# Kernel tuning notes

Measured on AMD Instinct MI355X. Metric: run time of the kernel, lower is better.

Reference implementation:

```python
import jax, jax.numpy as jnp
import numpy as np

Z_DIM = 256
N_MOD = 8
CAT = Z_DIM * N_MOD          # 2048
YS = 1024
B = 4096
EPS = 1e-5


def _layer_norm(x, g, b):
    mu = jnp.mean(x, axis=-1, keepdims=True)
    var = jnp.mean((x - mu) ** 2, axis=-1, keepdims=True)
    return (x - mu) * jax.lax.rsqrt(var + EPS) * g + b


def setup_inputs() -> dict:
    key = jax.random.key(0)
    ks = jax.random.split(key, 16)
    s_cat = 1.0 / np.sqrt(CAT)
    s_ys = 1.0 / np.sqrt(YS)
    return {
        "z_stack": jax.random.normal(ks[0], (N_MOD, B, Z_DIM), jnp.float32),
        "Wq": jax.random.normal(ks[1], (CAT, CAT), jnp.float32) * s_cat,
        "bq": jnp.zeros((CAT,), jnp.float32),
        "Wk": jax.random.normal(ks[2], (CAT, CAT), jnp.float32) * s_cat,
        "bk": jnp.zeros((CAT,), jnp.float32),
        "Wv": jax.random.normal(ks[3], (CAT, CAT), jnp.float32) * s_cat,
        "bv": jnp.zeros((CAT,), jnp.float32),
        "W1": jax.random.normal(ks[4], (CAT, YS), jnp.float32) * s_cat,
        "b1": jnp.zeros((YS,), jnp.float32),
        "W2": jax.random.normal(ks[5], (YS, CAT), jnp.float32) * s_ys,
        "b2": jnp.zeros((CAT,), jnp.float32),
        "ln1_g": jnp.ones((CAT,), jnp.float32),
        "ln1_b": jnp.zeros((CAT,), jnp.float32),
        "ln2_g": jnp.ones((CAT,), jnp.float32),
        "ln2_b": jnp.zeros((CAT,), jnp.float32),
        "Wys": jax.random.normal(ks[6], (CAT, YS), jnp.float32) * s_cat,
        "bys": jnp.zeros((YS,), jnp.float32),
        "Ws": jax.random.normal(ks[7], (N_MOD, YS, Z_DIM), jnp.float32) * s_ys,
        "bs": jnp.zeros((N_MOD, Z_DIM), jnp.float32),
    }


def reference(z_stack, Wq, bq, Wk, bk, Wv, bv, W1, b1, W2, b2,
              ln1_g, ln1_b, ln2_g, ln2_b, Wys, bys, Ws, bs):
    M, Bn, Zd = z_stack.shape
    # torch.cat(z, dim=1): [B, M*Zd]
    x = jnp.transpose(z_stack, (1, 0, 2)).reshape(Bn, M * Zd)
    # self-attention over the batch dim (unscaled, as in source)
    q = x @ Wq + bq
    k = x @ Wk + bk
    v = x @ Wv + bv
    attended = jax.nn.softmax(q @ k.T, axis=-1) @ v  # [B, B] scores
    # dropout is identity in eval mode
    x = _layer_norm(x + attended, ln1_g, ln1_b)
    h = jax.nn.gelu(x @ W1 + b1, approximate=False) @ W2 + b2
    h = _layer_norm(x + h, ln2_g, ln2_b)
    yb = h @ Wys + bys                               # [B, YS]
    # per-module scaling layers, stacked output [M, B, Zd]
    y = jnp.einsum('bs,msz->mbz', yb, Ws) + bs[:, None, :]
    return y
```

## Files before the change

kernel.cpp:

```cpp
#include <hip/hip_runtime.h>
#include <hip/hip_bf16.h>
#include <cstdint>
#include <cstddef>
#include <math.h>

typedef __bf16 bf16x8 __attribute__((ext_vector_type(8)));
typedef float  f32x4  __attribute__((ext_vector_type(4)));

#define DEVI __device__ __forceinline__

static constexpr int BB = 4096;
static constexpr int CD = 2048;
static constexpr int ZD = 256;

DEVI unsigned short f2bf(float f) {
  __bf16 h = (__bf16)f;
  return __builtin_bit_cast(unsigned short, h);
}
DEVI float bf2f(unsigned short u) {
  return (float)__builtin_bit_cast(__bf16, u);
}

DEVI void gload_lds16(const void* g, void* l) {
  __builtin_amdgcn_global_load_lds(
      (__attribute__((address_space(1))) void*)(g),
      (__attribute__((address_space(3))) void*)(l), 16, 0, 0);
}

DEVI int swz(int L) { return L ^ (((L >> 7) & 7) << 4); }

__global__ __launch_bounds__(256) void pack_x(
    const float* __restrict__ z, float* __restrict__ x,
    unsigned short* __restrict__ x2) {
  const int i = (blockIdx.x * 256 + threadIdx.x) * 4;
  const int m  = i >> 20;
  const int r  = i & 1048575;
  const int b  = r >> 8;
  const int zd = r & 255;
  const float4 v = *(const float4*)(z + i);
  const size_t o32 = (size_t)b * CD + m * ZD + zd;
  *(float4*)(x + o32) = v;
  ushort4 h, l;
  h.x = f2bf(v.x); l.x = f2bf(v.x - bf2f(h.x));
  h.y = f2bf(v.y); l.y = f2bf(v.y - bf2f(h.y));
  h.z = f2bf(v.z); l.z = f2bf(v.z - bf2f(h.z));
  h.w = f2bf(v.w); l.w = f2bf(v.w - bf2f(h.w));
  const size_t o2 = (size_t)b * 4096 + m * ZD + zd;
  *(ushort4*)(x2 + o2) = h;
  *(ushort4*)(x2 + o2 + 2048) = l;
}

template<bool LO>
__global__ void transpose_split(const float* __restrict__ in,
                                unsigned short* __restrict__ oh,
                                int R, int C, int ldo) {
  __shared__ float tile[32][33];
  const int c0 = blockIdx.x * 32, r0 = blockIdx.y * 32;
  const int tx = threadIdx.x, ty = threadIdx.y;
#pragma unroll
  for (int k = 0; k < 4; ++k)
    tile[ty + 8 * k][tx] = in[(size_t)(r0 + ty + 8 * k) * C + (c0 + tx)];
  __syncthreads();
#pragma unroll
  for (int k = 0; k < 4; ++k) {
    const float f = tile[tx][ty + 8 * k];
    const size_t o = (size_t)(c0 + ty + 8 * k) * ldo + (r0 + tx);
    const unsigned short h = f2bf(f);
    oh[o] = h;
    if constexpr (LO) oh[o + R] = f2bf(f - bf2f(h));
  }
}

__global__ void transpose_ws(const float* __restrict__ in,
                             unsigned short* __restrict__ outp) {
  __shared__ float tile[32][33];
  const int m = blockIdx.z;
  const float* src = in + (size_t)m * 262144;
  unsigned short* dst = outp + (size_t)m * 262144;
  const int c0 = blockIdx.x * 32, r0 = blockIdx.y * 32;
  const int tx = threadIdx.x, ty = threadIdx.y;
#pragma unroll
  for (int k = 0; k < 4; ++k)
    tile[ty + 8 * k][tx] = src[(size_t)(r0 + ty + 8 * k) * 256 + (c0 + tx)];
  __syncthreads();
#pragma unroll
  for (int k = 0; k < 4; ++k)
    dst[(size_t)(c0 + ty + 8 * k) * 1024 + (r0 + tx)] = f2bf(tile[tx][ty + 8 * k]);
}

__global__ void transpose_bf16(const unsigned short* __restrict__ in,
                               unsigned short* __restrict__ outp, int R, int C) {
  __shared__ unsigned short tile[32][33];
  const int c0 = blockIdx.x * 32, r0 = blockIdx.y * 32;
  const int tx = threadIdx.x, ty = threadIdx.y;
#pragma unroll
  for (int k = 0; k < 4; ++k)
    tile[ty + 8 * k][tx] = in[(size_t)(r0 + ty + 8 * k) * C + (c0 + tx)];
  __syncthreads();
#pragma unroll
  for (int k = 0; k < 4; ++k)
    outp[(size_t)(c0 + ty + 8 * k) * R + (r0 + tx)] = tile[tx][ty + 8 * k];
}

#define DOMFMA(QI, QJ, AF, BF)                                            \
  {                                                                       \
    _Pragma("unroll") for (int ks = 0; ks < 2; ++ks) {                    \
      _Pragma("unroll") for (int f = 0; f < 4; ++f) {                     \
        _Pragma("unroll") for (int g = 0; g < 2; ++g) {                   \
          acc[(QI) * 4 + f][(QJ) * 2 + g] =                               \
              __builtin_amdgcn_mfma_f32_16x16x32_bf16(                    \
                  AF[f][ks], BF[g][ks], acc[(QI) * 4 + f][(QJ) * 2 + g],  \
                  0, 0, 0);                                               \
        }                                                                 \
      }                                                                   \
    }                                                                     \
  }

#define PH_SYNC()                                         \
  do {                                                    \
    __builtin_amdgcn_s_barrier();                         \
    asm volatile("s_waitcnt lgkmcnt(0)" ::: "memory");    \
    __builtin_amdgcn_sched_barrier(0);                    \
    __builtin_amdgcn_s_setprio(1);                        \
  } while (0)

#define PH_END()                                          \
  do {                                                    \
    __builtin_amdgcn_s_setprio(0);                        \
    __builtin_amdgcn_sched_barrier(0);                    \
    __builtin_amdgcn_s_barrier();                         \
  } while (0)

template<int EP, bool SEG>
__global__ __launch_bounds__(512, 2) void gemm256(
    const unsigned short* __restrict__ A,
    const unsigned short* __restrict__ Bt,
    const float* __restrict__ bias, const float* __restrict__ bias2,
    float* __restrict__ Cf,
    unsigned short* __restrict__ Ob1, unsigned short* __restrict__ Ob2,
    int Kv, int lda, int ldb, int N, int nbx) {
  extern __shared__ char lds[];
  const int NK = Kv >> 6;
  const int t = threadIdx.x;
  const int lane = t & 63;
  const int w = t >> 6;
  const int wm = w >> 2, wn = w & 3;
  const int lr = lane & 15, kg = lane >> 4;
  const int q8 = gridDim.x >> 3;
  const int bid = (blockIdx.x & 7) * q8 + (blockIdx.x >> 3);
  const int bx = bid % nbx, by = bid / nbx;
  const int Ar0 = by * 256, Br0 = bx * 256;

  const int Lb = t << 4;
  const int rowL = Lb >> 7;
  const int colb = swz(Lb) & 127;
  const char* Abase = (const char*)A + (size_t)(Ar0 + rowL) * lda * 2 + colb;
  const char* Bbase = (const char*)Bt + (size_t)(Br0 + rowL) * ldb * 2 + colb;
  const size_t ldaB = (size_t)lda * 128;
  const size_t ldbB = (size_t)ldb * 128;
  char* const ldw = lds + ((t >> 6) << 10);

  auto stageA = [&](int c, int kk, int dst_off) {
    gload_lds16(Abase + (size_t)c * ldaB + ((unsigned)kk << 1), ldw + dst_off);
  };
  auto stageB = [&](int c, int kk, int dst_off) {
    gload_lds16(Bbase + (size_t)c * ldbB + ((unsigned)kk << 1), ldw + dst_off);
  };
  auto rdA = [&](const char* buf, int qi, int f, int ks) {
    const int L = swz(((qi * 64 + f * 16 + lr) << 7) + ks * 64 + kg * 16);
    return *(const bf16x8*)(buf + wm * 16384 + L);
  };
  auto rdB = [&](const char* buf, int qj, int g, int ks) {
    const int L = swz(((wn * 64 + qj * 32 + g * 16 + lr) << 7) + ks * 64 + kg * 16);
    return *(const bf16x8*)(buf + 32768 + L);
  };
  auto kA = [](int k0) { return SEG ? (k0 - ((k0 >> 11) == 2 ? 4096 : 0)) : k0; };
  auto kB = [](int k0) { return SEG ? (k0 - ((k0 >> 11) >= 1 ? 2048 : 0)) : k0; };

  f32x4 acc[8][4] = {};
  bf16x8 af[4][2], b0[2][2], b1[2][2];

  {
    stageA(0, kA(0), 0);
    stageA(1, kA(0), 8192);
    stageA(2, kA(0), 16384);
    stageA(3, kA(0), 24576);
    stageB(0, kB(0), 32768);
    stageB(1, kB(0), 40960);
    stageB(2, kB(0), 49152);
    stageB(3, kB(0), 57344);
    stageA(0, kA(64), 65536 + 0);
    stageA(2, kA(64), 65536 + 16384);
    stageB(0, kB(64), 65536 + 32768);
    stageB(1, kB(64), 65536 + 40960);
    stageB(2, kB(64), 65536 + 49152);
    stageB(3, kB(64), 65536 + 57344);
    asm volatile("s_waitcnt vmcnt(6)" ::: "memory");
    __builtin_amdgcn_sched_barrier(0);
    __builtin_amdgcn_s_barrier();
  }

  for (int tt = 0; tt < NK; ++tt) {
    const int cur = tt & 1;
    const char* buf = lds + cur * 65536;
    const int curo = cur * 65536, nxto = (cur ^ 1) * 65536;
    const int k1 = (tt + 1) * 64, k2 = (tt + 2) * 64;

#pragma unroll
    for (int f = 0; f < 4; ++f)
#pragma unroll
      for (int ks = 0; ks < 2; ++ks) af[f][ks] = rdA(buf, 0, f, ks);
#pragma unroll
    for (int g = 0; g < 2; ++g)
#pragma unroll
      for (int ks = 0; ks < 2; ++ks) b0[g][ks] = rdB(buf, 0, g, ks);
    if (tt + 1 < NK) {
      stageA(1, kA(k1), nxto + 8192);
      stageA(3, kA(k1), nxto + 24576);
    }
    asm volatile("s_waitcnt lgkmcnt(8)" ::: "memory");
    __builtin_amdgcn_sched_barrier(0);
    PH_SYNC();
    DOMFMA(0, 0, af, b0);
    PH_END();

#pragma unroll
    for (int g = 0; g < 2; ++g)
#pragma unroll
      for (int ks = 0; ks < 2; ++ks) b1[g][ks] = rdB(buf, 1, g, ks);
    if (tt + 2 < NK) {
      stageA(0, kA(k2), curo + 0);
      stageA(2, kA(k2), curo + 16384);
    }
    PH_SYNC();
    DOMFMA(0, 1, af, b1);
    PH_END();

#pragma unroll
    for (int f = 0; f < 4; ++f)
#pragma unroll
      for (int ks = 0; ks < 2; ++ks) af[f][ks] = rdA(buf, 1, f, ks);
    if (tt + 2 < NK) {
      stageB(0, kB(k2), curo + 32768);
      stageB(1, kB(k2), curo + 40960);
    }
    PH_SYNC();
    DOMFMA(1, 0, af, b0);
    PH_END();

    if (tt + 2 < NK) {
      stageB(2, kB(k2), curo + 49152);
      stageB(3, kB(k2), curo + 57344);
      asm volatile("s_waitcnt vmcnt(6)" ::: "memory");
    } else {
      asm volatile("s_waitcnt vmcnt(0)" ::: "memory");
    }
    __builtin_amdgcn_sched_barrier(0);
    PH_SYNC();
    DOMFMA(1, 1, af, b1);
    PH_END();
  }

  const int rbase = Ar0 + wm * 128 + kg * 4;
  const int cbase = Br0 + wn * 64 + lr;
#pragma unroll
  for (int rf = 0; rf < 8; ++rf) {
#pragma unroll
    for (int cf = 0; cf < 4; ++cf) {
      const int col = cbase + cf * 16;
#pragma unroll
      for (int q = 0; q < 4; ++q) {
        const int row = rbase + rf * 16 + q;
        float val = acc[rf][cf][q];
        if constexpr (EP == 0) {
          Cf[(size_t)row * N + col] = val;
        } else {
          if (col < 2048) {
            val += bias[col];
            const unsigned short h = f2bf(val);
            Ob1[(size_t)row * 4096 + col] = h;
            Ob1[(size_t)row * 4096 + 2048 + col] = f2bf(val - bf2f(h));
          } else {
            const int c2 = col - 2048;
            val += bias2[c2];
            const unsigned short h = f2bf(val);
            Ob2[(size_t)row * 4096 + c2] = h;
            Ob2[(size_t)row * 4096 + 2048 + c2] = f2bf(val - bf2f(h));
          }
        }
      }
    }
  }
}

template<int EP>
__global__ __launch_bounds__(256) void gemm_bt(
    const unsigned short* __restrict__ Ah,
    const unsigned short* __restrict__ Bh,
    const float* __restrict__ bias,
    float* __restrict__ Cf, unsigned short* __restrict__ Cb,
    int M, int N, int K, int lda, int ldb) {
  __shared__ unsigned short lds[2][128 * 32];
  const int t = threadIdx.x;
  const int lane = t & 63;
  const int w = t >> 6;
  const int wr = (w >> 1) * 64, wc = (w & 1) * 64;
  const int lr = lane & 15, kg = lane >> 4;
  const size_t Ar0 = (size_t)blockIdx.y * 128;
  const size_t Br0 = (size_t)blockIdx.x * 128;

  f32x4 acc[4][4] = {};

  for (int k0 = 0; k0 < K; k0 += 32) {
#pragma unroll
    for (int rnd = 0; rnd < 2; ++rnd) {
      const int e = t * 8 + rnd * 2048;
      const int row = e >> 5, col = e & 31;
      const size_t ga = (Ar0 + row) * (size_t)lda + (k0 + col);
      const size_t gb = (Br0 + row) * (size_t)ldb + (k0 + col);
      const int lo = (w << 9) + rnd * 2048;
      gload_lds16(Ah + ga, &lds[0][lo]);
      gload_lds16(Bh + gb, &lds[1][lo]);
    }
    __syncthreads();
    bf16x8 ah[4], bh[4];
#pragma unroll
    for (int i = 0; i < 4; ++i) {
      ah[i] = *(const bf16x8*)&lds[0][((wr + i * 16 + lr) << 5) + (kg << 3)];
      bh[i] = *(const bf16x8*)&lds[1][((wc + i * 16 + lr) << 5) + (kg << 3)];
    }
#pragma unroll
    for (int i = 0; i < 4; ++i)
#pragma unroll
      for (int j = 0; j < 4; ++j)
        acc[i][j] = __builtin_amdgcn_mfma_f32_16x16x32_bf16(ah[i], bh[j], acc[i][j], 0, 0, 0);
    __syncthreads();
  }

  const int rb = (int)Ar0 + wr + (lane >> 4) * 4;
  const int cb = (int)Br0 + wc + lr;
#pragma unroll
  for (int i = 0; i < 4; ++i) {
#pragma unroll
    for (int j = 0; j < 4; ++j) {
      const int col = cb + j * 16;
      const float bsv = bias ? bias[col] : 0.0f;
#pragma unroll
      for (int q = 0; q < 4; ++q) {
        const int row = rb + i * 16 + q;
        const float val = acc[i][j][q] + bsv;
        const size_t o = (size_t)row * N + col;
        if constexpr (EP == 0) {
          Cf[o] = val;
        } else if constexpr (EP == 1) {
          Cb[o] = f2bf(val);
        } else if constexpr (EP == 2) {
          const float ge = 0.5f * val * (1.0f + erff(val * 0.70710678118654752f));
          Cb[o] = f2bf(ge);
        } else {
          const size_t oo = (size_t)(col >> 8) * ((size_t)BB * ZD)
                          + (size_t)row * ZD + (col & 255);
          Cf[oo] = val;
        }
      }
    }
  }
}

__global__ __launch_bounds__(256) void softmax_rows(const float* __restrict__ S,
                                                    unsigned short* __restrict__ P) {
  const int row = blockIdx.x;
  const int t = threadIdx.x;
  const int lane = t & 63, w = t >> 6;
  const float* s = S + (size_t)row * 4096;
  float4 v[4];
  float mx = -3.4e38f;
#pragma unroll
  for (int i = 0; i < 4; ++i) {
    v[i] = *(const float4*)(s + (size_t)(t + 256 * i) * 4);
    mx = fmaxf(mx, fmaxf(fmaxf(v[i].x, v[i].y), fmaxf(v[i].z, v[i].w)));
  }
#pragma unroll
  for (int off = 32; off >= 1; off >>= 1) mx = fmaxf(mx, __shfl_xor(mx, off));
  __shared__ float redm[4], redsum[4];
  if (lane == 0) redm[w] = mx;
  __syncthreads();
  mx = fmaxf(fmaxf(redm[0], redm[1]), fmaxf(redm[2], redm[3]));
  float sum = 0.f;
#pragma unroll
  for (int i = 0; i < 4; ++i) {
    v[i].x = expf(v[i].x - mx);
    v[i].y = expf(v[i].y - mx);
    v[i].z = expf(v[i].z - mx);
    v[i].w = expf(v[i].w - mx);
    sum += v[i].x + v[i].y + v[i].z + v[i].w;
  }
#pragma unroll
  for (int off = 32; off >= 1; off >>= 1) sum += __shfl_xor(sum, off);
  if (lane == 0) redsum[w] = sum;
  __syncthreads();
  sum = redsum[0] + redsum[1] + redsum[2] + redsum[3];
  const float inv = 1.0f / sum;
  unsigned short* p = P + (size_t)row * 4096;
#pragma unroll
  for (int i = 0; i < 4; ++i) {
    ushort4 u;
    u.x = f2bf(v[i].x * inv);
    u.y = f2bf(v[i].y * inv);
    u.z = f2bf(v[i].z * inv);
    u.w = f2bf(v[i].w * inv);
    *(ushort4*)(p + (size_t)(t + 256 * i) * 4) = u;
  }
}

template<bool WF32>
__global__ __launch_bounds__(256) void ln_fused(
    const float* __restrict__ a, const float* __restrict__ b,
    const float* __restrict__ g, const float* __restrict__ be,
    float* __restrict__ of, unsigned short* __restrict__ ob) {
  const int row = blockIdx.x;
  const int t = threadIdx.x;
  const int lane = t & 63, w = t >> 6;
  const float* ar = a + (size_t)row * 2048;
  const float* br = b + (size_t)row * 2048;
  float4 x[2];
  float s = 0.f, ss = 0.f;
#pragma unroll
  for (int i = 0; i < 2; ++i) {
    const int o = (t + 256 * i) * 4;
    const float4 av = *(const float4*)(ar + o);
    const float4 bv = *(const float4*)(br + o);
    x[i].x = av.x + bv.x; x[i].y = av.y + bv.y;
    x[i].z = av.z + bv.z; x[i].w = av.w + bv.w;
    s  += x[i].x + x[i].y + x[i].z + x[i].w;
    ss += x[i].x * x[i].x + x[i].y * x[i].y + x[i].z * x[i].z + x[i].w * x[i].w;
  }
#pragma unroll
  for (int off = 32; off >= 1; off >>= 1) {
    s  += __shfl_xor(s, off);
    ss += __shfl_xor(ss, off);
  }
  __shared__ float rs[4], rss[4];
  if (lane == 0) { rs[w] = s; rss[w] = ss; }
  __syncthreads();
  s  = rs[0] + rs[1] + rs[2] + rs[3];
  ss = rss[0] + rss[1] + rss[2] + rss[3];
  const float mu  = s * (1.0f / 2048.0f);
  const float var = ss * (1.0f / 2048.0f) - mu * mu;
  const float inv = rsqrtf(var + 1e-5f);
#pragma unroll
  for (int i = 0; i < 2; ++i) {
    const int o = (t + 256 * i) * 4;
    const float4 gv  = *(const float4*)(g + o);
    const float4 bev = *(const float4*)(be + o);
    float4 y;
    y.x = (x[i].x - mu) * inv * gv.x + bev.x;
    y.y = (x[i].y - mu) * inv * gv.y + bev.y;
    y.z = (x[i].z - mu) * inv * gv.z + bev.z;
    y.w = (x[i].w - mu) * inv * gv.w + bev.w;
    if constexpr (WF32) *(float4*)(of + (size_t)row * 2048 + o) = y;
    ushort4 u;
    u.x = f2bf(y.x); u.y = f2bf(y.y); u.z = f2bf(y.z); u.w = f2bf(y.w);
    *(ushort4*)(ob + (size_t)row * 2048 + o) = u;
  }
}

extern "C" void kernel_launch(void* const* d_in, const int* in_sizes, int n_in,
                              void* d_out, int out_size, void* d_ws, size_t ws_size,
                              hipStream_t stream) {
  (void)in_sizes; (void)n_in; (void)out_size;
  const float* z    = (const float*)d_in[0];
  const float* Wq   = (const float*)d_in[1];
  const float* bq   = (const float*)d_in[2];
  const float* Wk   = (const float*)d_in[3];
  const float* bk   = (const float*)d_in[4];
  const float* Wv   = (const float*)d_in[5];
  const float* bv   = (const float*)d_in[6];
  const float* W1   = (const float*)d_in[7];
  const float* b1   = (const float*)d_in[8];
  const float* W2   = (const float*)d_in[9];
  const float* b2   = (const float*)d_in[10];
  const float* ln1g = (const float*)d_in[11];
  const float* ln1b = (const float*)d_in[12];
  const float* ln2g = (const float*)d_in[13];
  const float* ln2b = (const float*)d_in[14];
  const float* Wys  = (const float*)d_in[15];
  const float* bys  = (const float*)d_in[16];
  const float* Ws   = (const float*)d_in[17];
  const float* bs   = (const float*)d_in[18];
  float* out = (float*)d_out;
  char* ws = (char*)d_ws;

  const size_t MB = 1048576;
  const size_t off_x    = 0;
  const size_t off_h2   = 0;
  const size_t off_x2   = 32 * MB;
  const size_t off_Bqk  = 64 * MB;
  const size_t off_S    = 32 * MB;
  const size_t off_Aq   = 96 * MB;
  const size_t off_P    = 96 * MB;
  const size_t off_x1f  = 96 * MB;
  const size_t off_Btk  = 128 * MB;
  const size_t off_att  = 128 * MB;
  const size_t off_hmid = 128 * MB;
  const size_t off_ybbf = 136 * MB;
  const size_t off_Vbf  = 160 * MB;
  const size_t off_x1bf = 160 * MB;
  const size_t off_Vt   = 176 * MB;
  const size_t off_x2bf = 176 * MB;
  const size_t off_Wvt  = 192 * MB;
  const size_t off_W1t  = 200 * MB;
  const size_t off_W2t  = 204 * MB;
  const size_t off_Wyst = 208 * MB;
  const size_t off_Wst  = 212 * MB;
  if (ws_size < 216 * MB) return;

#define F32P(o) ((float*)(ws + (o)))
#define BFP(o)  ((unsigned short*)(ws + (o)))

  const dim3 tb(32, 8);
  const int LDSB = 131072;

  pack_x<<<8192, 256, 0, stream>>>(z, F32P(off_x), BFP(off_x2));
  transpose_split<true ><<<dim3(64, 64), tb, 0, stream>>>(Wq, BFP(off_Bqk), 2048, 2048, 4096);
  transpose_split<true ><<<dim3(64, 64), tb, 0, stream>>>(Wk, BFP(off_Bqk) + (size_t)2048 * 4096, 2048, 2048, 4096);
  transpose_split<false><<<dim3(64, 64), tb, 0, stream>>>(Wv, BFP(off_Wvt), 2048, 2048, 2048);
  transpose_split<false><<<dim3(32, 64), tb, 0, stream>>>(W1, BFP(off_W1t), 2048, 1024, 2048);
  transpose_split<false><<<dim3(64, 32), tb, 0, stream>>>(W2, BFP(off_W2t), 1024, 2048, 1024);
  transpose_split<false><<<dim3(32, 64), tb, 0, stream>>>(Wys, BFP(off_Wyst), 2048, 1024, 2048);
  transpose_ws<<<dim3(8, 32, 8), tb, 0, stream>>>(Ws, BFP(off_Wst));

  gemm_bt<1><<<dim3(16, 32), 256, 0, stream>>>(BFP(off_x2), BFP(off_Wvt), bv,
      nullptr, BFP(off_Vbf), 4096, 2048, 2048, 4096, 2048);
  transpose_bf16<<<dim3(64, 128), tb, 0, stream>>>(BFP(off_Vbf), BFP(off_Vt), 4096, 2048);

  gemm256<1, true ><<<256, 512, LDSB, stream>>>(BFP(off_x2), BFP(off_Bqk), bq, bk,
      nullptr, BFP(off_Aq), BFP(off_Btk), 6144, 4096, 4096, 4096, 16);

  gemm256<0, true ><<<256, 512, LDSB, stream>>>(BFP(off_Aq), BFP(off_Btk), nullptr, nullptr,
      F32P(off_S), nullptr, nullptr, 6144, 4096, 4096, 4096, 16);

  softmax_rows<<<4096, 256, 0, stream>>>(F32P(off_S), BFP(off_P));
  gemm_bt<0><<<dim3(16, 32), 256, 0, stream>>>(BFP(off_P), BFP(off_Vt), nullptr,
      F32P(off_att), nullptr, 4096, 2048, 4096, 4096, 4096);
  ln_fused<true ><<<4096, 256, 0, stream>>>(F32P(off_x), F32P(off_att), ln1g, ln1b,
      F32P(off_x1f), BFP(off_x1bf));

  gemm_bt<2><<<dim3(8, 32), 256, 0, stream>>>(BFP(off_x1bf), BFP(off_W1t), b1,
      nullptr, BFP(off_hmid), 4096, 1024, 2048, 2048, 2048);
  gemm_bt<0><<<dim3(16, 32), 256, 0, stream>>>(BFP(off_hmid), BFP(off_W2t), b2,
      F32P(off_h2), nullptr, 4096, 2048, 1024, 1024, 1024);
  ln_fused<false><<<4096, 256, 0, stream>>>(F32P(off_x1f), F32P(off_h2), ln2g, ln2b,
      nullptr, BFP(off_x2bf));

  gemm_bt<1><<<dim3(8, 32), 256, 0, stream>>>(BFP(off_x2bf), BFP(off_Wyst), bys,
      nullptr, BFP(off_ybbf), 4096, 1024, 2048, 2048, 2048);
  gemm_bt<4><<<dim3(16, 32), 256, 0, stream>>>(BFP(off_ybbf), BFP(off_Wst), bs,
      out, nullptr, 4096, 2048, 1024, 1024, 1024);
}
```

Baseline: 785.9 us.

## Merge weight transposes, compute V transposed directly, drop fp32 x copy, remap tiles

```diff
diff --git a/kernel.cpp b/kernel.cpp
--- a/kernel.cpp
+++ b/kernel.cpp
@@ -10,7 +10,6 @@
 #define DEVI __device__ __forceinline__
 
 static constexpr int BB = 4096;
-static constexpr int CD = 2048;
 static constexpr int ZD = 256;
 
 DEVI unsigned short f2bf(float f) {
@@ -30,16 +29,13 @@
 DEVI int swz(int L) { return L ^ (((L >> 7) & 7) << 4); }
 
 __global__ __launch_bounds__(256) void pack_x(
-    const float* __restrict__ z, float* __restrict__ x,
-    unsigned short* __restrict__ x2) {
+    const float* __restrict__ z, unsigned short* __restrict__ x2) {
   const int i = (blockIdx.x * 256 + threadIdx.x) * 4;
   const int m  = i >> 20;
   const int r  = i & 1048575;
   const int b  = r >> 8;
   const int zd = r & 255;
   const float4 v = *(const float4*)(z + i);
-  const size_t o32 = (size_t)b * CD + m * ZD + zd;
-  *(float4*)(x + o32) = v;
   ushort4 h, l;
   h.x = f2bf(v.x); l.x = f2bf(v.x - bf2f(h.x));
   h.y = f2bf(v.y); l.y = f2bf(v.y - bf2f(h.y));
@@ -50,56 +46,49 @@
   *(ushort4*)(x2 + o2 + 2048) = l;
 }
 
-template<bool LO>
-__global__ void transpose_split(const float* __restrict__ in,
-                                unsigned short* __restrict__ oh,
-                                int R, int C, int ldo) {
+__global__ __launch_bounds__(256) void transpose_all(
+    const float* __restrict__ Wq, const float* __restrict__ Wk,
+    const float* __restrict__ Wv, const float* __restrict__ W1,
+    const float* __restrict__ W2, const float* __restrict__ Wys,
+    const float* __restrict__ Ws,
+    unsigned short* __restrict__ Bqk, unsigned short* __restrict__ Wvt,
+    unsigned short* __restrict__ W1t, unsigned short* __restrict__ W2t,
+    unsigned short* __restrict__ Wyst, unsigned short* __restrict__ Wst) {
   __shared__ float tile[32][33];
-  const int c0 = blockIdx.x * 32, r0 = blockIdx.y * 32;
+  int b = blockIdx.x;
+  const float* src;
+  unsigned short* dh;
+  int C, ldo, nbx, loff = 0;
+  if (b < 8192) {
+    const int which = b >> 12; b &= 4095;
+    src = which ? Wk : Wq;
+    dh = Bqk + (size_t)which * 2048 * 4096;
+    C = 2048; ldo = 4096; nbx = 64; loff = 2048;
+  } else if (b < 12288) { b -= 8192;  src = Wv;  dh = Wvt;  C = 2048; ldo = 2048; nbx = 64; }
+  else if (b < 14336)   { b -= 12288; src = W1;  dh = W1t;  C = 1024; ldo = 2048; nbx = 32; }
+  else if (b < 16384)   { b -= 14336; src = W2;  dh = W2t;  C = 2048; ldo = 1024; nbx = 64; }
+  else if (b < 18432)   { b -= 16384; src = Wys; dh = Wyst; C = 1024; ldo = 2048; nbx = 32; }
+  else {
+    b -= 18432;
+    const int m = b >> 8; b &= 255;
+    src = Ws + (size_t)m * 262144;
+    dh = Wst + (size_t)m * 262144;
+    C = 256; ldo = 1024; nbx = 8;
+  }
+  const int c0 = (b % nbx) * 32, r0 = (b / nbx) * 32;
   const int tx = threadIdx.x, ty = threadIdx.y;
 #pragma unroll
   for (int k = 0; k < 4; ++k)
-    tile[ty + 8 * k][tx] = in[(size_t)(r0 + ty + 8 * k) * C + (c0 + tx)];
+    tile[ty + 8 * k][tx] = src[(size_t)(r0 + ty + 8 * k) * C + (c0 + tx)];
   __syncthreads();
 #pragma unroll
   for (int k = 0; k < 4; ++k) {
     const float f = tile[tx][ty + 8 * k];
     const size_t o = (size_t)(c0 + ty + 8 * k) * ldo + (r0 + tx);
     const unsigned short h = f2bf(f);
-    oh[o] = h;
-    if constexpr (LO) oh[o + R] = f2bf(f - bf2f(h));
-  }
-}
-
-__global__ void transpose_ws(const float* __restrict__ in,
-                             unsigned short* __restrict__ outp) {
-  __shared__ float tile[32][33];
-  const int m = blockIdx.z;
-  const float* src = in + (size_t)m * 262144;
-  unsigned short* dst = outp + (size_t)m * 262144;
-  const int c0 = blockIdx.x * 32, r0 = blockIdx.y * 32;
-  const int tx = threadIdx.x, ty = threadIdx.y;
-#pragma unroll
-  for (int k = 0; k < 4; ++k)
-    tile[ty + 8 * k][tx] = src[(size_t)(r0 + ty + 8 * k) * 256 + (c0 + tx)];
-  __syncthreads();
-#pragma unroll
-  for (int k = 0; k < 4; ++k)
-    dst[(size_t)(c0 + ty + 8 * k) * 1024 + (r0 + tx)] = f2bf(tile[tx][ty + 8 * k]);
-}
-
-__global__ void transpose_bf16(const unsigned short* __restrict__ in,
-                               unsigned short* __restrict__ outp, int R, int C) {
-  __shared__ unsigned short tile[32][33];
-  const int c0 = blockIdx.x * 32, r0 = blockIdx.y * 32;
-  const int tx = threadIdx.x, ty = threadIdx.y;
-#pragma unroll
-  for (int k = 0; k < 4; ++k)
-    tile[ty + 8 * k][tx] = in[(size_t)(r0 + ty + 8 * k) * C + (c0 + tx)];
-  __syncthreads();
-#pragma unroll
-  for (int k = 0; k < 4; ++k)
-    outp[(size_t)(c0 + ty + 8 * k) * R + (r0 + tx)] = tile[tx][ty + 8 * k];
+    dh[o] = h;
+    if (loff) dh[o + loff] = f2bf(f - bf2f(h));
+  }
 }
 
 #define DOMFMA(QI, QJ, AF, BF)                                            \
@@ -146,9 +135,16 @@
   const int w = t >> 6;
   const int wm = w >> 2, wn = w & 3;
   const int lr = lane & 15, kg = lane >> 4;
-  const int q8 = gridDim.x >> 3;
-  const int bid = (blockIdx.x & 7) * q8 + (blockIdx.x >> 3);
-  const int bx = bid % nbx, by = bid / nbx;
+  int bx, by;
+  if (gridDim.x == 256 && nbx == 16) {
+    const int xcd = blockIdx.x & 7, i = blockIdx.x >> 3;
+    by = (xcd >> 1) * 4 + (i >> 3);
+    bx = (xcd & 1) * 8 + (i & 7);
+  } else {
+    const int q8 = gridDim.x >> 3;
+    const int bid = (blockIdx.x & 7) * q8 + (blockIdx.x >> 3);
+    bx = bid % nbx; by = bid / nbx;
+  }
   const int Ar0 = by * 256, Br0 = bx * 256;
 
   const int Lb = t << 4;
@@ -344,7 +340,7 @@
 #pragma unroll
     for (int j = 0; j < 4; ++j) {
       const int col = cb + j * 16;
-      const float bsv = bias ? bias[col] : 0.0f;
+      const float bsv = (EP == 5) ? 0.0f : (bias ? bias[col] : 0.0f);
 #pragma unroll
       for (int q = 0; q < 4; ++q) {
         const int row = rb + i * 16 + q;
@@ -357,10 +353,12 @@
         } else if constexpr (EP == 2) {
           const float ge = 0.5f * val * (1.0f + erff(val * 0.70710678118654752f));
           Cb[o] = f2bf(ge);
-        } else {
+        } else if constexpr (EP == 4) {
           const size_t oo = (size_t)(col >> 8) * ((size_t)BB * ZD)
                           + (size_t)row * ZD + (col & 255);
           Cf[oo] = val;
+        } else {
+          Cb[o] = f2bf(val + bias[row]);
         }
       }
     }
@@ -413,7 +411,7 @@
   }
 }
 
-template<bool WF32>
+template<bool ZG, bool WF32>
 __global__ __launch_bounds__(256) void ln_fused(
     const float* __restrict__ a, const float* __restrict__ b,
     const float* __restrict__ g, const float* __restrict__ be,
@@ -421,14 +419,18 @@
   const int row = blockIdx.x;
   const int t = threadIdx.x;
   const int lane = t & 63, w = t >> 6;
-  const float* ar = a + (size_t)row * 2048;
   const float* br = b + (size_t)row * 2048;
   float4 x[2];
   float s = 0.f, ss = 0.f;
 #pragma unroll
   for (int i = 0; i < 2; ++i) {
     const int o = (t + 256 * i) * 4;
-    const float4 av = *(const float4*)(ar + o);
+    float4 av;
+    if constexpr (ZG) {
+      av = *(const float4*)(a + ((size_t)(o >> 8) * 4096 + row) * 256 + (o & 255));
+    } else {
+      av = *(const float4*)(a + (size_t)row * 2048 + o);
+    }
     const float4 bv = *(const float4*)(br + o);
     x[i].x = av.x + bv.x; x[i].y = av.y + bv.y;
     x[i].z = av.z + bv.z; x[i].w = av.w + bv.w;
@@ -492,7 +494,6 @@
   char* ws = (char*)d_ws;
 
   const size_t MB = 1048576;
-  const size_t off_x    = 0;
   const size_t off_h2   = 0;
   const size_t off_x2   = 32 * MB;
   const size_t off_Bqk  = 64 * MB;
@@ -504,7 +505,6 @@
   const size_t off_att  = 128 * MB;
   const size_t off_hmid = 128 * MB;
   const size_t off_ybbf = 136 * MB;
-  const size_t off_Vbf  = 160 * MB;
   const size_t off_x1bf = 160 * MB;
   const size_t off_Vt   = 176 * MB;
   const size_t off_x2bf = 176 * MB;
@@ -518,21 +518,14 @@
 #define F32P(o) ((float*)(ws + (o)))
 #define BFP(o)  ((unsigned short*)(ws + (o)))
 
-  const dim3 tb(32, 8);
   const int LDSB = 131072;
 
-  pack_x<<<8192, 256, 0, stream>>>(z, F32P(off_x), BFP(off_x2));
-  transpose_split<true ><<<dim3(64, 64), tb, 0, stream>>>(Wq, BFP(off_Bqk), 2048, 2048, 4096);
-  transpose_split<true ><<<dim3(64, 64), tb, 0, stream>>>(Wk, BFP(off_Bqk) + (size_t)2048 * 4096, 2048, 2048, 4096);
-  transpose_split<false><<<dim3(64, 64), tb, 0, stream>>>(Wv, BFP(off_Wvt), 2048, 2048, 2048);
-  transpose_split<false><<<dim3(32, 64), tb, 0, stream>>>(W1, BFP(off_W1t), 2048, 1024, 2048);
-  transpose_split<false><<<dim3(64, 32), tb, 0, stream>>>(W2, BFP(off_W2t), 1024, 2048, 1024);
-  transpose_split<false><<<dim3(32, 64), tb, 0, stream>>>(Wys, BFP(off_Wyst), 2048, 1024, 2048);
-  transpose_ws<<<dim3(8, 32, 8), tb, 0, stream>>>(Ws, BFP(off_Wst));
-
-  gemm_bt<1><<<dim3(16, 32), 256, 0, stream>>>(BFP(off_x2), BFP(off_Wvt), bv,
-      nullptr, BFP(off_Vbf), 4096, 2048, 2048, 4096, 2048);
-  transpose_bf16<<<dim3(64, 128), tb, 0, stream>>>(BFP(off_Vbf), BFP(off_Vt), 4096, 2048);
+  pack_x<<<8192, 256, 0, stream>>>(z, BFP(off_x2));
+  transpose_all<<<20480, dim3(32, 8), 0, stream>>>(Wq, Wk, Wv, W1, W2, Wys, Ws,
+      BFP(off_Bqk), BFP(off_Wvt), BFP(off_W1t), BFP(off_W2t), BFP(off_Wyst), BFP(off_Wst));
+
+  gemm_bt<5><<<dim3(32, 16), 256, 0, stream>>>(BFP(off_Wvt), BFP(off_x2), bv,
+      nullptr, BFP(off_Vt), 2048, 4096, 2048, 2048, 4096);
 
   gemm256<1, true ><<<256, 512, LDSB, stream>>>(BFP(off_x2), BFP(off_Bqk), bq, bk,
       nullptr, BFP(off_Aq), BFP(off_Btk), 6144, 4096, 4096, 4096, 16);
@@ -543,14 +536,14 @@
   softmax_rows<<<4096, 256, 0, stream>>>(F32P(off_S), BFP(off_P));
   gemm_bt<0><<<dim3(16, 32), 256, 0, stream>>>(BFP(off_P), BFP(off_Vt), nullptr,
       F32P(off_att), nullptr, 4096, 2048, 4096, 4096, 4096);
-  ln_fused<true ><<<4096, 256, 0, stream>>>(F32P(off_x), F32P(off_att), ln1g, ln1b,
+  ln_fused<true, true ><<<4096, 256, 0, stream>>>(z, F32P(off_att), ln1g, ln1b,
       F32P(off_x1f), BFP(off_x1bf));
 
   gemm_bt<2><<<dim3(8, 32), 256, 0, stream>>>(BFP(off_x1bf), BFP(off_W1t), b1,
       nullptr, BFP(off_hmid), 4096, 1024, 2048, 2048, 2048);
   gemm_bt<0><<<dim3(16, 32), 256, 0, stream>>>(BFP(off_hmid), BFP(off_W2t), b2,
       F32P(off_h2), nullptr, 4096, 2048, 1024, 1024, 1024);
-  ln_fused<false><<<4096, 256, 0, stream>>>(F32P(off_x1f), F32P(off_h2), ln2g, ln2b,
+  ln_fused<false, false><<<4096, 256, 0, stream>>>(F32P(off_x1f), F32P(off_h2), ln2g, ln2b,
       nullptr, BFP(off_x2bf));
 
   gemm_bt<1><<<dim3(8, 32), 256, 0, stream>>>(BFP(off_x2bf), BFP(off_Wyst), bys,
```

Result: faster. 757.8 us (-3.6%).
